# Kernel optimization log

Hardware: AMD Instinct MI355X
Metric: run time of the kernel (lower is better)

Reference implementation:

```python
import jax, jax.numpy as jnp
import numpy as np
from jax import lax

R = 8  # REGION_NUM_

def _avgpool3(x):
    # AvgPool2d(kernel=H-2*(H//3), stride=H//3) -> exactly 3x3 spatial output
    H = x.shape[2]
    s = H // 3
    k = H - 2 * s
    y = lax.reduce_window(x, 0.0, lax.add, (1, 1, k, k), (1, 1, s, s), 'VALID')
    return y / float(k * k)

def _hist_drconv(x, hist, wa, ba, wb, bb, out_ch):
    # x: [B,Cin,H,W], hist: [B,R,H,W]
    B, Cin, H, W = x.shape
    p = _avgpool3(x)                                                     # [B,Cin,3,3]
    h = jax.nn.sigmoid(jnp.einsum('bchw,oc->bohw', p, wa) + ba[None, :, None, None])  # [B,R*R,3,3]
    hg = h.reshape(B, R, R, 3, 3)
    wbg = wb.reshape(R, Cin * out_ch, R)                                 # grouped 1x1 conv, groups=R
    kern = jnp.einsum('brchw,roc->brohw', hg, wbg) + bb.reshape(1, R, Cin * out_ch, 1, 1)
    ki = kern.reshape(B, R * out_ch, Cin, 3, 3)                          # per-sample dynamic kernels
    def per_sample(xi, kb):
        # xi: [Cin,H,W], kb: [R*out,Cin,3,3] -> [R*out,H,W]
        return lax.conv_general_dilated(xi[None], kb, (1, 1), [(1, 1), (1, 1)])[0]
    y = jax.vmap(per_sample)(x, ki)                                      # [B,R*out,H,W]
    y = y.reshape(B, R, out_ch, H, W)
    # asign_index: one-hot of argmax over regions, select-sum
    mask = jax.nn.one_hot(jnp.argmax(hist, axis=1), R, axis=1, dtype=y.dtype)  # [B,R,H,W]
    return (y * mask[:, :, None]).sum(axis=1)                            # [B,out,H,W]

def _bn_relu(y, g, b, m, v):
    scale = (g / jnp.sqrt(v + 1e-5))[None, :, None, None]
    return jax.nn.relu((y - m[None, :, None, None]) * scale + b[None, :, None, None])

def setup_inputs() -> dict:
    key = jax.random.key(0)
    ks = jax.random.split(key, 20)
    B, Cin, Cmid, Cout, H = 8, 8, 8, 8, 256
    f32 = jnp.float32
    d = {}
    d['x'] = jax.random.normal(ks[0], (B, Cin, H, H), f32)
    d['histmap'] = jax.random.uniform(ks[1], (B, R, H, H), dtype=f32)
    d['w1a'] = jax.random.normal(ks[2], (R * R, Cin), f32) * 0.1
    d['b1a'] = jax.random.normal(ks[3], (R * R,), f32) * 0.1
    d['w1b'] = jax.random.normal(ks[4], (R * Cin * Cmid, R), f32) * 0.1
    d['b1b'] = jax.random.normal(ks[5], (R * Cin * Cmid,), f32) * 0.1
    d['g1'] = jax.random.uniform(ks[6], (Cmid,), dtype=f32) + 0.5
    d['be1'] = jax.random.normal(ks[7], (Cmid,), f32) * 0.1
    d['m1'] = jax.random.normal(ks[8], (Cmid,), f32) * 0.1
    d['v1'] = jax.random.uniform(ks[9], (Cmid,), dtype=f32) + 0.5
    d['w2a'] = jax.random.normal(ks[10], (R * R, Cmid), f32) * 0.1
    d['b2a'] = jax.random.normal(ks[11], (R * R,), f32) * 0.1
    d['w2b'] = jax.random.normal(ks[12], (R * Cmid * Cout, R), f32) * 0.1
    d['b2b'] = jax.random.normal(ks[13], (R * Cmid * Cout,), f32) * 0.1
    d['g2'] = jax.random.uniform(ks[14], (Cout,), dtype=f32) + 0.5
    d['be2'] = jax.random.normal(ks[15], (Cout,), f32) * 0.1
    d['m2'] = jax.random.normal(ks[16], (Cout,), f32) * 0.1
    d['v2'] = jax.random.uniform(ks[17], (Cout,), dtype=f32) + 0.5
    return d

def reference(x, histmap, w1a, b1a, w1b, b1b, g1, be1, m1, v1,
              w2a, b2a, w2b, b2b, g2, be2, m2, v2):
    y = _hist_drconv(x, histmap, w1a, b1a, w1b, b1b, 8)
    y = _bn_relu(y, g1, be1, m1, v1)
    y = _hist_drconv(y, histmap, w2a, b2a, w2b, b2b, 8)
    return _bn_relu(y, g2, be2, m2, v2)
```

## Files before the change

kernel.cpp:

```cpp
#include <hip/hip_runtime.h>
#include <math.h>


#define HWPX 65536
#define HDIM 256

typedef __fp16 h2 __attribute__((ext_vector_type(2)));

#if defined(__has_builtin) && __has_builtin(__builtin_amdgcn_fdot2)
__device__ __forceinline__ float fdot2(h2 a, h2 b, float c) {
  return __builtin_amdgcn_fdot2(a, b, c, false);
}
#else
__device__ __forceinline__ float fdot2(h2 a, h2 b, float c) {
  return c + (float)a[0] * (float)b[0] + (float)a[1] * (float)b[1];
}
#endif

union UH { uint u; h2 h; };
union U4H { uint4 u4; h2 h[4]; };

__global__ __launch_bounds__(256) void prep_kernel(const float* __restrict__ x,
                                                   const float* __restrict__ hist,
                                                   float* __restrict__ rs1,
                                                   uint* __restrict__ xh,
                                                   unsigned char* __restrict__ regmap) {
  int u = blockIdx.x;
  int t = threadIdx.x;
  int wave = t >> 6, lane = t & 63;
  if (u < 2048) {
    int cp = u & 3, rg = (u >> 2) & 63, b = u >> 8;
    int row = rg * 4 + wave;
    const float* pa = x + ((size_t)(b * 8 + 2 * cp) * HWPX) + row * HDIM + lane * 4;
    const float4 va = *(const float4*)pa;
    const float4 vb = *(const float4*)(pa + HWPX);
    U4H pk;
    pk.h[0] = __builtin_amdgcn_cvt_pkrtz(va.x, vb.x);
    pk.h[1] = __builtin_amdgcn_cvt_pkrtz(va.y, vb.y);
    pk.h[2] = __builtin_amdgcn_cvt_pkrtz(va.z, vb.z);
    pk.h[3] = __builtin_amdgcn_cvt_pkrtz(va.w, vb.w);
    *(uint4*)(xh + (size_t)(b * 4 + cp) * HWPX + row * HDIM + lane * 4) = pk.u4;
    float a0 = 0.f, a1 = 0.f, a2 = 0.f, b0 = 0.f, b1 = 0.f, b2 = 0.f;
#pragma unroll
    for (int p = 0; p < 4; p++) {
      int px = lane * 4 + p;
      float fa = (&va.x)[p], fb = (&vb.x)[p];
      if (px <= 85)  { a0 += fa; b0 += fb; }
      if (px >= 85 && px <= 170) { a1 += fa; b1 += fb; }
      if (px >= 170) { a2 += fa; b2 += fb; }
    }
#pragma unroll
    for (int off = 32; off >= 1; off >>= 1) {
      a0 += __shfl_xor(a0, off); a1 += __shfl_xor(a1, off); a2 += __shfl_xor(a2, off);
      b0 += __shfl_xor(b0, off); b1 += __shfl_xor(b1, off); b2 += __shfl_xor(b2, off);
    }
    if (lane == 0) {
      float* qa = rs1 + ((size_t)(b * 8 + 2 * cp) * 256 + row) * 3;
      qa[0] = a0; qa[1] = a1; qa[2] = a2;
      float* qb = qa + 768;
      qb[0] = b0; qb[1] = b1; qb[2] = b2;
    }
  } else {
    int u2 = u - 2048;
    int b = u2 >> 6, rg = u2 & 63;
    int row = rg * 4 + wave;
    int x0 = lane * 4;
    const float* hp = hist + (size_t)b * 8 * HWPX + row * HDIM + x0;
    float4 hv[8];
#pragma unroll
    for (int r = 0; r < 8; r++) hv[r] = *(const float4*)(hp + (size_t)r * HWPX);
    uchar4 rg4;
#pragma unroll
    for (int p = 0; p < 4; p++) {
      float best = (&hv[0].x)[p];
      int reg = 0;
#pragma unroll
      for (int r = 1; r < 8; r++) {
        float q = (&hv[r].x)[p];
        if (q > best) { best = q; reg = r; }
      }
      (&rg4.x)[p] = (unsigned char)reg;
    }
    *(uchar4*)(regmap + (size_t)b * HWPX + row * HDIM + x0) = rg4;
  }
}

template <int LAYER>
__global__ __launch_bounds__(256) void conv_kernel(
    const uint* __restrict__ xh, const unsigned char* __restrict__ regmap,
    const float* __restrict__ rs,
    const float* __restrict__ wa, const float* __restrict__ ba,
    const float* __restrict__ wb, const float* __restrict__ bb,
    const float* __restrict__ g, const float* __restrict__ be,
    const float* __restrict__ m, const float* __restrict__ v,
    uint* __restrict__ outh, float* __restrict__ outf,
    float* __restrict__ rs2out) {
  __shared__ uint KsU[8 * 292];
  __shared__ float pp[72][3];
  __shared__ float pP[8][9];
  __shared__ float hh[576];
  __shared__ float bns[8], bnsh[8];

  int bid = blockIdx.x;
  int b = bid & 7;
  int rg = bid >> 3;
  int wave = threadIdx.x >> 6, lane = threadIdx.x & 63;
  int row = rg * 4 + wave;
  int x0 = lane * 4;
  int t = threadIdx.x;

  if (t < 216) {
    int u = t / 3, part = t - 3 * (t / 3);
    int c = u / 9, ij = u % 9, i = ij / 3, j = ij % 3;
    int r0 = 85 * i + part * 29;
    int cnt = (part == 2) ? 28 : 29;
    const float* q = rs + ((size_t)(b * 8 + c) * 256 + r0) * 3 + j;
    float s = 0.f;
    for (int k = 0; k < cnt; k++) s += q[k * 3];
    pp[u][part] = s;
  }
  if (t >= 248) {
    int oc = t - 248;
    float s = g[oc] * rsqrtf(v[oc] + 1e-5f);
    bns[oc] = s;
    bnsh[oc] = be[oc] - m[oc] * s;
  }
  __syncthreads();
  if (t < 72) pP[t / 9][t % 9] = (pp[t][0] + pp[t][1] + pp[t][2]) * (1.f / 7396.f);
  __syncthreads();
  for (int u = t; u < 576; u += 256) {
    int o = u / 9, ij = u - o * 9;
    float z = ba[o];
#pragma unroll
    for (int c = 0; c < 8; c++) z += pP[c][ij] * wa[o * 8 + c];
    hh[u] = 1.f / (1.f + expf(-z));
  }
  __syncthreads();
  {
    int reg = t >> 5, z = t & 31, oc = z >> 2, q = z & 3;
    int row0 = reg * 64 + oc * 8 + q * 2;
    const float* w0p = wb + row0 * 8;
    float4 wA  = *(const float4*)(w0p);
    float4 wA2 = *(const float4*)(w0p + 4);
    float4 wB  = *(const float4*)(w0p + 8);
    float4 wB2 = *(const float4*)(w0p + 12);
    float bb0 = bb[row0], bb1 = bb[row0 + 1];
    const float* hp = hh + reg * 72;
#pragma unroll
    for (int tap = 0; tap < 9; tap++) {
      float v0 = bb0, v1 = bb1;
#pragma unroll
      for (int cc = 0; cc < 4; cc++) {
        float hv = hp[cc * 9 + tap];
        v0 += hv * (&wA.x)[cc];
        v1 += hv * (&wB.x)[cc];
      }
#pragma unroll
      for (int cc = 0; cc < 4; cc++) {
        float hv = hp[(4 + cc) * 9 + tap];
        v0 += hv * (&wA2.x)[cc];
        v1 += hv * (&wB2.x)[cc];
      }
      UH pk;
      pk.h[0] = (__fp16)v0;
      pk.h[1] = (__fp16)v1;
      KsU[reg * 292 + tap * 32 + z] = pk.u;
    }
  }
  __syncthreads();

  uint win[4][3][6];
#pragma unroll
  for (int cp = 0; cp < 4; cp++) {
    const uint* plane = xh + (size_t)(b * 4 + cp) * HWPX;
#pragma unroll
    for (int dy = 0; dy < 3; dy++) {
      int yy = row + dy - 1;
      if ((unsigned)yy < 256u) {
        const uint* rp = plane + yy * HDIM + x0;
        uint4 mv = *(const uint4*)rp;
        win[cp][dy][0] = (x0 > 0) ? rp[-1] : 0u;
        win[cp][dy][1] = mv.x; win[cp][dy][2] = mv.y;
        win[cp][dy][3] = mv.z; win[cp][dy][4] = mv.w;
        win[cp][dy][5] = (x0 < 252) ? rp[4] : 0u;
      } else {
#pragma unroll
        for (int q = 0; q < 6; q++) win[cp][dy][q] = 0u;
      }
    }
  }

  uchar4 rg4 = *(const uchar4*)(regmap + (size_t)b * HWPX + row * HDIM + x0);

  float acc[4][8];
#pragma unroll
  for (int p = 0; p < 4; p++)
#pragma unroll
    for (int oc = 0; oc < 8; oc++) acc[p][oc] = 0.f;

#pragma unroll
  for (int p = 0; p < 4; p++) {
    int reg = (&rg4.x)[p];
    const char* Kr = (const char*)KsU + reg * 1168;
#pragma unroll
    for (int di = 0; di < 3; di++) {
#pragma unroll
      for (int dj = 0; dj < 3; dj++) {
        UH w0, w1, w2, w3;
        w0.u = win[0][di][p + dj];
        w1.u = win[1][di][p + dj];
        w2.u = win[2][di][p + dj];
        w3.u = win[3][di][p + dj];
        const char* kt = Kr + (di * 3 + dj) * 128;
#pragma unroll
        for (int oc = 0; oc < 8; oc++) {
          U4H kw;
          kw.u4 = *(const uint4*)(kt + oc * 16);
          float a = acc[p][oc];
          a = fdot2(w0.h, kw.h[0], a);
          a = fdot2(w1.h, kw.h[1], a);
          a = fdot2(w2.h, kw.h[2], a);
          a = fdot2(w3.h, kw.h[3], a);
          acc[p][oc] = a;
        }
      }
    }
  }

#pragma unroll
  for (int p = 0; p < 4; p++)
#pragma unroll
    for (int oc = 0; oc < 8; oc++)
      acc[p][oc] = fmaxf(acc[p][oc] * bns[oc] + bnsh[oc], 0.f);

  if (LAYER == 1) {
#pragma unroll
    for (int cp = 0; cp < 4; cp++) {
      U4H pk;
#pragma unroll
      for (int p = 0; p < 4; p++)
        pk.h[p] = __builtin_amdgcn_cvt_pkrtz(acc[p][2 * cp], acc[p][2 * cp + 1]);
      *(uint4*)(outh + (size_t)(b * 4 + cp) * HWPX + row * HDIM + x0) = pk.u4;
    }
#pragma unroll
    for (int oc = 0; oc < 8; oc++) {
      float s0 = 0.f, s1 = 0.f, s2 = 0.f;
#pragma unroll
      for (int p = 0; p < 4; p++) {
        int px = x0 + p;
        float val = acc[p][oc];
        if (px <= 85) s0 += val;
        if (px >= 85 && px <= 170) s1 += val;
        if (px >= 170) s2 += val;
      }
#pragma unroll
      for (int off = 32; off >= 1; off >>= 1) {
        s0 += __shfl_xor(s0, off);
        s1 += __shfl_xor(s1, off);
        s2 += __shfl_xor(s2, off);
      }
      if (lane == 0) {
        float* q = rs2out + ((size_t)(b * 8 + oc) * 256 + row) * 3;
        q[0] = s0; q[1] = s1; q[2] = s2;
      }
    }
  } else {
#pragma unroll
    for (int oc = 0; oc < 8; oc++) {
      float4 o4 = make_float4(acc[0][oc], acc[1][oc], acc[2][oc], acc[3][oc]);
      *(float4*)(outf + (size_t)(b * 8 + oc) * HWPX + row * HDIM + x0) = o4;
    }
  }
}

extern "C" void kernel_launch(void* const* d_in, const int* in_sizes, int n_in,
                              void* d_out, int out_size, void* d_ws, size_t ws_size,
                              hipStream_t stream) {
  const float* x    = (const float*)d_in[0];
  const float* hist = (const float*)d_in[1];
  const float* w1a  = (const float*)d_in[2];
  const float* b1a  = (const float*)d_in[3];
  const float* w1b  = (const float*)d_in[4];
  const float* b1b  = (const float*)d_in[5];
  const float* g1   = (const float*)d_in[6];
  const float* be1  = (const float*)d_in[7];
  const float* m1   = (const float*)d_in[8];
  const float* v1   = (const float*)d_in[9];
  const float* w2a  = (const float*)d_in[10];
  const float* b2a  = (const float*)d_in[11];
  const float* w2b  = (const float*)d_in[12];
  const float* b2b  = (const float*)d_in[13];
  const float* g2   = (const float*)d_in[14];
  const float* be2  = (const float*)d_in[15];
  const float* m2   = (const float*)d_in[16];
  const float* v2   = (const float*)d_in[17];
  float* outp = (float*)d_out;

  char* ws = (char*)d_ws;
  unsigned char* regmap = (unsigned char*)ws;
  uint* xh  = (uint*)(ws + 524288);
  uint* y1h = (uint*)(ws + 8912896);
  float* rs1 = (float*)(ws + 17301504);
  float* rs2 = (float*)(ws + 17399808);

  prep_kernel<<<2560, 256, 0, stream>>>(x, hist, rs1, xh, regmap);
  conv_kernel<1><<<512, 256, 0, stream>>>(xh, regmap, rs1, w1a, b1a, w1b, b1b,
                                          g1, be1, m1, v1, y1h, nullptr, rs2);
  conv_kernel<2><<<512, 256, 0, stream>>>(y1h, regmap, rs2, w2a, b2a, w2b, b2b,
                                          g2, be2, m2, v2, nullptr, outp, nullptr);
}
```

Before: 55.72 us.

## Fuse prep and both conv layers into one persistent kernel with grid barriers

Merges the three launches into a single persistent kernel of 512 blocks that loops over the prep work, then runs layer-1 and layer-2 convolution phases separated by atomic-counter grid barriers. The goal is to remove kernel launch gaps and the tail drain between dependent stages. It adds a memset launch for the barrier counters and relies on all 512 blocks being co-resident, which an ordinary launch does not guarantee. Barrier spinning and fewer prep blocks in flight could also cost time.

```diff
diff --git a/kernel.cpp b/kernel.cpp
--- a/kernel.cpp
+++ b/kernel.cpp
@@ -4,6 +4,7 @@
 
 #define HWPX 65536
 #define HDIM 256
+#define NBLK 512u
 
 typedef __fp16 h2 __attribute__((ext_vector_type(2)));
 
@@ -20,13 +21,31 @@
 union UH { uint u; h2 h; };
 union U4H { uint4 u4; h2 h[4]; };
 
-__global__ __launch_bounds__(256) void prep_kernel(const float* __restrict__ x,
-                                                   const float* __restrict__ hist,
-                                                   float* __restrict__ rs1,
-                                                   uint* __restrict__ xh,
-                                                   unsigned char* __restrict__ regmap) {
-  int u = blockIdx.x;
-  int t = threadIdx.x;
+struct ConvSmem {
+  uint KsU[8 * 292];
+  float pp[72][3];
+  float pP[8][9];
+  float hh[576];
+  float bns[8], bnsh[8];
+};
+
+__device__ __forceinline__ void gridbar(uint* cnt, uint target) {
+  __syncthreads();
+  if (threadIdx.x == 0) {
+    __threadfence();
+    atomicAdd(cnt, 1u);
+    while (atomicAdd(cnt, 0u) < target) __builtin_amdgcn_s_sleep(8);
+  }
+  __syncthreads();
+  __threadfence();
+}
+
+__device__ __forceinline__ void prep_unit(int u, int t,
+                                          const float* __restrict__ x,
+                                          const float* __restrict__ hist,
+                                          float* __restrict__ rs1,
+                                          uint* __restrict__ xh,
+                                          unsigned char* __restrict__ regmap) {
   int wave = t >> 6, lane = t & 63;
   if (u < 2048) {
     int cp = u & 3, rg = (u >> 2) & 63, b = u >> 8;
@@ -86,7 +105,8 @@
 }
 
 template <int LAYER>
-__global__ __launch_bounds__(256) void conv_kernel(
+__device__ __forceinline__ void conv_phase(
+    ConvSmem& sm, int bid, int t,
     const uint* __restrict__ xh, const unsigned char* __restrict__ regmap,
     const float* __restrict__ rs,
     const float* __restrict__ wa, const float* __restrict__ ba,
@@ -95,19 +115,11 @@
     const float* __restrict__ m, const float* __restrict__ v,
     uint* __restrict__ outh, float* __restrict__ outf,
     float* __restrict__ rs2out) {
-  __shared__ uint KsU[8 * 292];
-  __shared__ float pp[72][3];
-  __shared__ float pP[8][9];
-  __shared__ float hh[576];
-  __shared__ float bns[8], bnsh[8];
-
-  int bid = blockIdx.x;
   int b = bid & 7;
   int rg = bid >> 3;
-  int wave = threadIdx.x >> 6, lane = threadIdx.x & 63;
+  int wave = t >> 6, lane = t & 63;
   int row = rg * 4 + wave;
   int x0 = lane * 4;
-  int t = threadIdx.x;
 
   if (t < 216) {
     int u = t / 3, part = t - 3 * (t / 3);
@@ -117,23 +129,23 @@
     const float* q = rs + ((size_t)(b * 8 + c) * 256 + r0) * 3 + j;
     float s = 0.f;
     for (int k = 0; k < cnt; k++) s += q[k * 3];
-    pp[u][part] = s;
+    sm.pp[u][part] = s;
   }
   if (t >= 248) {
     int oc = t - 248;
     float s = g[oc] * rsqrtf(v[oc] + 1e-5f);
-    bns[oc] = s;
-    bnsh[oc] = be[oc] - m[oc] * s;
-  }
-  __syncthreads();
-  if (t < 72) pP[t / 9][t % 9] = (pp[t][0] + pp[t][1] + pp[t][2]) * (1.f / 7396.f);
+    sm.bns[oc] = s;
+    sm.bnsh[oc] = be[oc] - m[oc] * s;
+  }
+  __syncthreads();
+  if (t < 72) sm.pP[t / 9][t % 9] = (sm.pp[t][0] + sm.pp[t][1] + sm.pp[t][2]) * (1.f / 7396.f);
   __syncthreads();
   for (int u = t; u < 576; u += 256) {
     int o = u / 9, ij = u - o * 9;
     float z = ba[o];
 #pragma unroll
-    for (int c = 0; c < 8; c++) z += pP[c][ij] * wa[o * 8 + c];
-    hh[u] = 1.f / (1.f + expf(-z));
+    for (int c = 0; c < 8; c++) z += sm.pP[c][ij] * wa[o * 8 + c];
+    sm.hh[u] = 1.f / (1.f + expf(-z));
   }
   __syncthreads();
   {
@@ -145,7 +157,7 @@
     float4 wB  = *(const float4*)(w0p + 8);
     float4 wB2 = *(const float4*)(w0p + 12);
     float bb0 = bb[row0], bb1 = bb[row0 + 1];
-    const float* hp = hh + reg * 72;
+    const float* hp = sm.hh + reg * 72;
 #pragma unroll
     for (int tap = 0; tap < 9; tap++) {
       float v0 = bb0, v1 = bb1;
@@ -164,7 +176,7 @@
       UH pk;
       pk.h[0] = (__fp16)v0;
       pk.h[1] = (__fp16)v1;
-      KsU[reg * 292 + tap * 32 + z] = pk.u;
+      sm.KsU[reg * 292 + tap * 32 + z] = pk.u;
     }
   }
   __syncthreads();
@@ -201,7 +213,7 @@
 #pragma unroll
   for (int p = 0; p < 4; p++) {
     int reg = (&rg4.x)[p];
-    const char* Kr = (const char*)KsU + reg * 1168;
+    const char* Kr = (const char*)sm.KsU + reg * 1168;
 #pragma unroll
     for (int di = 0; di < 3; di++) {
 #pragma unroll
@@ -231,7 +243,7 @@
   for (int p = 0; p < 4; p++)
 #pragma unroll
     for (int oc = 0; oc < 8; oc++)
-      acc[p][oc] = fmaxf(acc[p][oc] * bns[oc] + bnsh[oc], 0.f);
+      acc[p][oc] = fmaxf(acc[p][oc] * sm.bns[oc] + sm.bnsh[oc], 0.f);
 
   if (LAYER == 1) {
 #pragma unroll
@@ -271,6 +283,33 @@
       *(float4*)(outf + (size_t)(b * 8 + oc) * HWPX + row * HDIM + x0) = o4;
     }
   }
+}
+
+__global__ __launch_bounds__(256, 2) void fused_kernel(
+    const float* __restrict__ x, const float* __restrict__ hist,
+    const float* __restrict__ w1a, const float* __restrict__ b1a,
+    const float* __restrict__ w1b, const float* __restrict__ b1b,
+    const float* __restrict__ g1, const float* __restrict__ be1,
+    const float* __restrict__ m1, const float* __restrict__ v1,
+    const float* __restrict__ w2a, const float* __restrict__ b2a,
+    const float* __restrict__ w2b, const float* __restrict__ b2b,
+    const float* __restrict__ g2, const float* __restrict__ be2,
+    const float* __restrict__ m2, const float* __restrict__ v2,
+    float* __restrict__ outp, unsigned char* __restrict__ regmap,
+    uint* __restrict__ xh, uint* __restrict__ y1h,
+    float* __restrict__ rs1, float* __restrict__ rs2,
+    uint* __restrict__ bar) {
+  __shared__ ConvSmem sm;
+  int bid = blockIdx.x;
+  int t = threadIdx.x;
+
+  for (int u = bid; u < 2560; u += 512) prep_unit(u, t, x, hist, rs1, xh, regmap);
+  gridbar(bar + 0, NBLK);
+  conv_phase<1>(sm, bid, t, xh, regmap, rs1, w1a, b1a, w1b, b1b,
+                g1, be1, m1, v1, y1h, nullptr, rs2);
+  gridbar(bar + 16, NBLK);
+  conv_phase<2>(sm, bid, t, y1h, regmap, rs2, w2a, b2a, w2b, b2b,
+                g2, be2, m2, v2, nullptr, outp, nullptr);
 }
 
 extern "C" void kernel_launch(void* const* d_in, const int* in_sizes, int n_in,
@@ -302,10 +341,18 @@
   uint* y1h = (uint*)(ws + 8912896);
   float* rs1 = (float*)(ws + 17301504);
   float* rs2 = (float*)(ws + 17399808);
-
-  prep_kernel<<<2560, 256, 0, stream>>>(x, hist, rs1, xh, regmap);
-  conv_kernel<1><<<512, 256, 0, stream>>>(xh, regmap, rs1, w1a, b1a, w1b, b1b,
-                                          g1, be1, m1, v1, y1h, nullptr, rs2);
-  conv_kernel<2><<<512, 256, 0, stream>>>(y1h, regmap, rs2, w2a, b2a, w2b, b2b,
-                                          g2, be2, m2, v2, nullptr, outp, nullptr);
-}
+  uint* bar  = (uint*)(ws + 17498112);
+
+  hipMemsetAsync(bar, 0, 128, stream);
+
+  void* args[] = {
+    (void*)&x, (void*)&hist,
+    (void*)&w1a, (void*)&b1a, (void*)&w1b, (void*)&b1b,
+    (void*)&g1, (void*)&be1, (void*)&m1, (void*)&v1,
+    (void*)&w2a, (void*)&b2a, (void*)&w2b, (void*)&b2b,
+    (void*)&g2, (void*)&be2, (void*)&m2, (void*)&v2,
+    (void*)&outp, (void*)&regmap, (void*)&xh, (void*)&y1h,
+    (void*)&rs1, (void*)&rs2, (void*)&bar,
+  };
+  hipLaunchKernel((const void*)fused_kernel, dim3(512), dim3(256), args, 0, stream);
+}
```

Result: slower. 191.7 us (+244.1%).

## Halve per-thread pixels, double conv grid, and hoist window loads before kernel build

Applied to the files above, without the earlier changes.

Each thread now computes 2 pixels instead of 4, with two waves covering a row, so the conv grid doubles to 1024 blocks and occupancy should rise under launch_bounds(256,4). The input-window and region-map loads move ahead of the per-block dynamic-kernel construction so their latency overlaps that setup work. Row-sum partials from the two half-row waves are combined through shared memory. The cost is that each block rebuilds its dynamic kernels for half as many pixels, doubling that redundant setup overall.

```diff
diff --git a/kernel.cpp b/kernel.cpp
--- a/kernel.cpp
+++ b/kernel.cpp
@@ -86,7 +86,7 @@
 }
 
 template <int LAYER>
-__global__ __launch_bounds__(256) void conv_kernel(
+__global__ __launch_bounds__(256, 4) void conv_kernel(
     const uint* __restrict__ xh, const unsigned char* __restrict__ regmap,
     const float* __restrict__ rs,
     const float* __restrict__ wa, const float* __restrict__ ba,
@@ -100,14 +100,38 @@
   __shared__ float pP[8][9];
   __shared__ float hh[576];
   __shared__ float bns[8], bnsh[8];
+  __shared__ float wred[4][8][3];
 
   int bid = blockIdx.x;
   int b = bid & 7;
   int rg = bid >> 3;
-  int wave = threadIdx.x >> 6, lane = threadIdx.x & 63;
-  int row = rg * 4 + wave;
-  int x0 = lane * 4;
   int t = threadIdx.x;
+  int wave = t >> 6, lane = t & 63;
+  int row = rg * 2 + (wave >> 1);
+  int x0 = (wave & 1) * 128 + lane * 2;
+
+  uint win[4][3][4];
+#pragma unroll
+  for (int cp = 0; cp < 4; cp++) {
+    const uint* plane = xh + (size_t)(b * 4 + cp) * HWPX;
+#pragma unroll
+    for (int dy = 0; dy < 3; dy++) {
+      int yy = row + dy - 1;
+      if ((unsigned)yy < 256u) {
+        const uint* rp = plane + yy * HDIM + x0;
+        uint2 mv = *(const uint2*)rp;
+        win[cp][dy][0] = (x0 > 0) ? rp[-1] : 0u;
+        win[cp][dy][1] = mv.x;
+        win[cp][dy][2] = mv.y;
+        win[cp][dy][3] = (x0 < 254) ? rp[2] : 0u;
+      } else {
+#pragma unroll
+        for (int q = 0; q < 4; q++) win[cp][dy][q] = 0u;
+      }
+    }
+  }
+  const unsigned char* rmp = regmap + (size_t)b * HWPX + row * HDIM + x0;
+  int reg0 = rmp[0], reg1 = rmp[1];
 
   if (t < 216) {
     int u = t / 3, part = t - 3 * (t / 3);
@@ -169,38 +193,15 @@
   }
   __syncthreads();
 
-  uint win[4][3][6];
-#pragma unroll
-  for (int cp = 0; cp < 4; cp++) {
-    const uint* plane = xh + (size_t)(b * 4 + cp) * HWPX;
-#pragma unroll
-    for (int dy = 0; dy < 3; dy++) {
-      int yy = row + dy - 1;
-      if ((unsigned)yy < 256u) {
-        const uint* rp = plane + yy * HDIM + x0;
-        uint4 mv = *(const uint4*)rp;
-        win[cp][dy][0] = (x0 > 0) ? rp[-1] : 0u;
-        win[cp][dy][1] = mv.x; win[cp][dy][2] = mv.y;
-        win[cp][dy][3] = mv.z; win[cp][dy][4] = mv.w;
-        win[cp][dy][5] = (x0 < 252) ? rp[4] : 0u;
-      } else {
-#pragma unroll
-        for (int q = 0; q < 6; q++) win[cp][dy][q] = 0u;
-      }
-    }
-  }
-
-  uchar4 rg4 = *(const uchar4*)(regmap + (size_t)b * HWPX + row * HDIM + x0);
-
-  float acc[4][8];
-#pragma unroll
-  for (int p = 0; p < 4; p++)
+  float acc[2][8];
+#pragma unroll
+  for (int p = 0; p < 2; p++)
 #pragma unroll
     for (int oc = 0; oc < 8; oc++) acc[p][oc] = 0.f;
 
 #pragma unroll
-  for (int p = 0; p < 4; p++) {
-    int reg = (&rg4.x)[p];
+  for (int p = 0; p < 2; p++) {
+    int reg = p ? reg1 : reg0;
     const char* Kr = (const char*)KsU + reg * 1168;
 #pragma unroll
     for (int di = 0; di < 3; di++) {
@@ -228,7 +229,7 @@
   }
 
 #pragma unroll
-  for (int p = 0; p < 4; p++)
+  for (int p = 0; p < 2; p++)
 #pragma unroll
     for (int oc = 0; oc < 8; oc++)
       acc[p][oc] = fmaxf(acc[p][oc] * bns[oc] + bnsh[oc], 0.f);
@@ -236,17 +237,18 @@
   if (LAYER == 1) {
 #pragma unroll
     for (int cp = 0; cp < 4; cp++) {
-      U4H pk;
-#pragma unroll
-      for (int p = 0; p < 4; p++)
-        pk.h[p] = __builtin_amdgcn_cvt_pkrtz(acc[p][2 * cp], acc[p][2 * cp + 1]);
-      *(uint4*)(outh + (size_t)(b * 4 + cp) * HWPX + row * HDIM + x0) = pk.u4;
+      uint2 pk;
+      UH h0, h1;
+      h0.h = __builtin_amdgcn_cvt_pkrtz(acc[0][2 * cp], acc[0][2 * cp + 1]);
+      h1.h = __builtin_amdgcn_cvt_pkrtz(acc[1][2 * cp], acc[1][2 * cp + 1]);
+      pk.x = h0.u; pk.y = h1.u;
+      *(uint2*)(outh + (size_t)(b * 4 + cp) * HWPX + row * HDIM + x0) = pk;
     }
 #pragma unroll
     for (int oc = 0; oc < 8; oc++) {
       float s0 = 0.f, s1 = 0.f, s2 = 0.f;
 #pragma unroll
-      for (int p = 0; p < 4; p++) {
+      for (int p = 0; p < 2; p++) {
         int px = x0 + p;
         float val = acc[p][oc];
         if (px <= 85) s0 += val;
@@ -259,16 +261,20 @@
         s1 += __shfl_xor(s1, off);
         s2 += __shfl_xor(s2, off);
       }
-      if (lane == 0) {
-        float* q = rs2out + ((size_t)(b * 8 + oc) * 256 + row) * 3;
-        q[0] = s0; q[1] = s1; q[2] = s2;
-      }
+      if (lane == 0) { wred[wave][oc][0] = s0; wred[wave][oc][1] = s1; wred[wave][oc][2] = s2; }
+    }
+    __syncthreads();
+    if (t < 48) {
+      int row_sub = t / 24, rem = t - row_sub * 24;
+      int oc = rem / 3, j = rem - 3 * oc;
+      float s = wred[row_sub * 2][oc][j] + wred[row_sub * 2 + 1][oc][j];
+      rs2out[((size_t)(b * 8 + oc) * 256 + (rg * 2 + row_sub)) * 3 + j] = s;
     }
   } else {
 #pragma unroll
     for (int oc = 0; oc < 8; oc++) {
-      float4 o4 = make_float4(acc[0][oc], acc[1][oc], acc[2][oc], acc[3][oc]);
-      *(float4*)(outf + (size_t)(b * 8 + oc) * HWPX + row * HDIM + x0) = o4;
+      float2 o2 = make_float2(acc[0][oc], acc[1][oc]);
+      *(float2*)(outf + (size_t)(b * 8 + oc) * HWPX + row * HDIM + x0) = o2;
     }
   }
 }
@@ -304,8 +310,8 @@
   float* rs2 = (float*)(ws + 17399808);
 
   prep_kernel<<<2560, 256, 0, stream>>>(x, hist, rs1, xh, regmap);
-  conv_kernel<1><<<512, 256, 0, stream>>>(xh, regmap, rs1, w1a, b1a, w1b, b1b,
-                                          g1, be1, m1, v1, y1h, nullptr, rs2);
-  conv_kernel<2><<<512, 256, 0, stream>>>(y1h, regmap, rs2, w2a, b2a, w2b, b2b,
-                                          g2, be2, m2, v2, nullptr, outp, nullptr);
-}
+  conv_kernel<1><<<1024, 256, 0, stream>>>(xh, regmap, rs1, w1a, b1a, w1b, b1b,
+                                           g1, be1, m1, v1, y1h, nullptr, rs2);
+  conv_kernel<2><<<1024, 256, 0, stream>>>(y1h, regmap, rs2, w2a, b2a, w2b, b2b,
+                                           g2, be2, m2, v2, nullptr, outp, nullptr);
+}
```

After: 62.78 us. +12.7%, slower.

## Compute dynamic region conv with MFMA over all regions and select via LDS

Applied to the files above, without the earlier changes.

Activations move to a channel-interleaved NHWC fp16 layout (8 channels per 16-byte word), and the conv kernel now stages six input rows in shared memory. Each wave then runs the 3x3 conv as an implicit GEMM with 16x16x32 f16 MFMA across all 64 region×channel outputs, picking the per-pixel region's outputs from an LDS staging buffer. This trades per-pixel fdot2 loops for matrix-core throughput at the cost of computing all 8 regions (8x redundant FLOPs) plus extra LDS traffic. The prep kernel now packs all 8 channels per block, and layer-2 output stores become scalar per pixel.

```diff
diff --git a/kernel.cpp b/kernel.cpp
--- a/kernel.cpp
+++ b/kernel.cpp
@@ -5,66 +5,63 @@
 #define HWPX 65536
 #define HDIM 256
 
-typedef __fp16 h2 __attribute__((ext_vector_type(2)));
-
-#if defined(__has_builtin) && __has_builtin(__builtin_amdgcn_fdot2)
-__device__ __forceinline__ float fdot2(h2 a, h2 b, float c) {
-  return __builtin_amdgcn_fdot2(a, b, c, false);
-}
-#else
-__device__ __forceinline__ float fdot2(h2 a, h2 b, float c) {
-  return c + (float)a[0] * (float)b[0] + (float)a[1] * (float)b[1];
-}
-#endif
-
-union UH { uint u; h2 h; };
-union U4H { uint4 u4; h2 h[4]; };
+typedef __fp16 h2v __attribute__((ext_vector_type(2)));
+typedef __fp16 v8h __attribute__((ext_vector_type(8)));
+typedef float v4f __attribute__((ext_vector_type(4)));
+
+union UH { uint u; h2v h; };
+union U4V8 { uint4 u4; v8h h8; };
 
 __global__ __launch_bounds__(256) void prep_kernel(const float* __restrict__ x,
                                                    const float* __restrict__ hist,
                                                    float* __restrict__ rs1,
-                                                   uint* __restrict__ xh,
+                                                   uint4* __restrict__ xh4,
                                                    unsigned char* __restrict__ regmap) {
-  int u = blockIdx.x;
-  int t = threadIdx.x;
-  int wave = t >> 6, lane = t & 63;
-  if (u < 2048) {
-    int cp = u & 3, rg = (u >> 2) & 63, b = u >> 8;
-    int row = rg * 4 + wave;
-    const float* pa = x + ((size_t)(b * 8 + 2 * cp) * HWPX) + row * HDIM + lane * 4;
-    const float4 va = *(const float4*)pa;
-    const float4 vb = *(const float4*)(pa + HWPX);
-    U4H pk;
-    pk.h[0] = __builtin_amdgcn_cvt_pkrtz(va.x, vb.x);
-    pk.h[1] = __builtin_amdgcn_cvt_pkrtz(va.y, vb.y);
-    pk.h[2] = __builtin_amdgcn_cvt_pkrtz(va.z, vb.z);
-    pk.h[3] = __builtin_amdgcn_cvt_pkrtz(va.w, vb.w);
-    *(uint4*)(xh + (size_t)(b * 4 + cp) * HWPX + row * HDIM + lane * 4) = pk.u4;
-    float a0 = 0.f, a1 = 0.f, a2 = 0.f, b0 = 0.f, b1 = 0.f, b2 = 0.f;
+  int u = blockIdx.x, t = threadIdx.x, w = t >> 6, l = t & 63;
+  if (u < 512) {
+    int b = u & 7, rg = u >> 3;
+    int row = rg * 4 + w;
+    const float* base = x + (size_t)b * 8 * HWPX + row * HDIM + l * 4;
+    float4 ch[8];
+#pragma unroll
+    for (int c = 0; c < 8; c++) ch[c] = *(const float4*)(base + (size_t)c * HWPX);
+    uint4* dst = xh4 + ((size_t)b * 256 + row) * 256 + l * 4;
 #pragma unroll
     for (int p = 0; p < 4; p++) {
-      int px = lane * 4 + p;
-      float fa = (&va.x)[p], fb = (&vb.x)[p];
-      if (px <= 85)  { a0 += fa; b0 += fb; }
-      if (px >= 85 && px <= 170) { a1 += fa; b1 += fb; }
-      if (px >= 170) { a2 += fa; b2 += fb; }
-    }
-#pragma unroll
-    for (int off = 32; off >= 1; off >>= 1) {
-      a0 += __shfl_xor(a0, off); a1 += __shfl_xor(a1, off); a2 += __shfl_xor(a2, off);
-      b0 += __shfl_xor(b0, off); b1 += __shfl_xor(b1, off); b2 += __shfl_xor(b2, off);
-    }
-    if (lane == 0) {
-      float* qa = rs1 + ((size_t)(b * 8 + 2 * cp) * 256 + row) * 3;
-      qa[0] = a0; qa[1] = a1; qa[2] = a2;
-      float* qb = qa + 768;
-      qb[0] = b0; qb[1] = b1; qb[2] = b2;
+      UH h0, h1, h2, h3;
+      h0.h = __builtin_amdgcn_cvt_pkrtz((&ch[0].x)[p], (&ch[1].x)[p]);
+      h1.h = __builtin_amdgcn_cvt_pkrtz((&ch[2].x)[p], (&ch[3].x)[p]);
+      h2.h = __builtin_amdgcn_cvt_pkrtz((&ch[4].x)[p], (&ch[5].x)[p]);
+      h3.h = __builtin_amdgcn_cvt_pkrtz((&ch[6].x)[p], (&ch[7].x)[p]);
+      dst[p] = make_uint4(h0.u, h1.u, h2.u, h3.u);
+    }
+#pragma unroll
+    for (int c = 0; c < 8; c++) {
+      float s0 = 0.f, s1 = 0.f, s2 = 0.f;
+#pragma unroll
+      for (int p = 0; p < 4; p++) {
+        int px = l * 4 + p;
+        float val = (&ch[c].x)[p];
+        if (px <= 85) s0 += val;
+        if (px >= 85 && px <= 170) s1 += val;
+        if (px >= 170) s2 += val;
+      }
+#pragma unroll
+      for (int off = 32; off >= 1; off >>= 1) {
+        s0 += __shfl_xor(s0, off);
+        s1 += __shfl_xor(s1, off);
+        s2 += __shfl_xor(s2, off);
+      }
+      if (l == 0) {
+        float* q = rs1 + ((size_t)(b * 8 + c) * 256 + row) * 3;
+        q[0] = s0; q[1] = s1; q[2] = s2;
+      }
     }
   } else {
-    int u2 = u - 2048;
-    int b = u2 >> 6, rg = u2 & 63;
-    int row = rg * 4 + wave;
-    int x0 = lane * 4;
+    int u2 = u - 512;
+    int b = u2 & 7, rg = u2 >> 3;
+    int row = rg * 4 + w;
+    int x0 = l * 4;
     const float* hp = hist + (size_t)b * 8 * HWPX + row * HDIM + x0;
     float4 hv[8];
 #pragma unroll
@@ -86,8 +83,8 @@
 }
 
 template <int LAYER>
-__global__ __launch_bounds__(256) void conv_kernel(
-    const uint* __restrict__ xh, const unsigned char* __restrict__ regmap,
+__global__ __launch_bounds__(256, 2) void conv_kernel(
+    const uint4* __restrict__ in4, const unsigned char* __restrict__ regmap,
     const float* __restrict__ rs,
     const float* __restrict__ wa, const float* __restrict__ ba,
     const float* __restrict__ wb, const float* __restrict__ bb,
@@ -95,26 +92,38 @@
     const float* __restrict__ m, const float* __restrict__ v,
     uint* __restrict__ outh, float* __restrict__ outf,
     float* __restrict__ rs2out) {
-  __shared__ uint KsU[8 * 292];
+  __shared__ uint4 xs[6][260];
+  __shared__ __align__(16) float Dbuf[4][64][20];
+  __shared__ uint4 Bf[4][3][64];
   __shared__ float pp[72][3];
   __shared__ float pP[8][9];
   __shared__ float hh[576];
   __shared__ float bns[8], bnsh[8];
+  __shared__ unsigned char rm[4][256];
 
   int bid = blockIdx.x;
-  int b = bid & 7;
-  int rg = bid >> 3;
-  int wave = threadIdx.x >> 6, lane = threadIdx.x & 63;
-  int row = rg * 4 + wave;
-  int x0 = lane * 4;
-  int t = threadIdx.x;
+  int b = bid & 7, rg = bid >> 3, r0 = rg * 4;
+  int t = threadIdx.x, w = t >> 6, l = t & 63;
+
+  for (int i = t; i < 6 * 256; i += 256) {
+    int dy = i >> 8, px = i & 255;
+    int yy = r0 - 1 + dy;
+    uint4 val = make_uint4(0, 0, 0, 0);
+    if ((unsigned)yy < 256u) val = in4[((size_t)b * 256 + yy) * 256 + px];
+    xs[dy][px + 1] = val;
+  }
+  if (t < 12) {
+    int rr = t % 6, cc = (t < 6) ? 0 : 257;
+    xs[rr][cc] = make_uint4(0, 0, 0, 0);
+  }
+  ((uint*)rm)[t] = *(const uint*)(regmap + (size_t)b * HWPX + (r0 + (t >> 6)) * HDIM + (t & 63) * 4);
 
   if (t < 216) {
     int u = t / 3, part = t - 3 * (t / 3);
     int c = u / 9, ij = u % 9, i = ij / 3, j = ij % 3;
-    int r0 = 85 * i + part * 29;
+    int rr0 = 85 * i + part * 29;
     int cnt = (part == 2) ? 28 : 29;
-    const float* q = rs + ((size_t)(b * 8 + c) * 256 + r0) * 3 + j;
+    const float* q = rs + ((size_t)(b * 8 + c) * 256 + rr0) * 3 + j;
     float s = 0.f;
     for (int k = 0; k < cnt; k++) s += q[k * 3];
     pp[u][part] = s;
@@ -137,138 +146,111 @@
   }
   __syncthreads();
   {
-    int reg = t >> 5, z = t & 31, oc = z >> 2, q = z & 3;
-    int row0 = reg * 64 + oc * 8 + q * 2;
-    const float* w0p = wb + row0 * 8;
-    float4 wA  = *(const float4*)(w0p);
-    float4 wA2 = *(const float4*)(w0p + 4);
-    float4 wB  = *(const float4*)(w0p + 8);
-    float4 wB2 = *(const float4*)(w0p + 12);
-    float bb0 = bb[row0], bb1 = bb[row0 + 1];
-    const float* hp = hh + reg * 72;
-#pragma unroll
-    for (int tap = 0; tap < 9; tap++) {
-      float v0 = bb0, v1 = bb1;
-#pragma unroll
-      for (int cc = 0; cc < 4; cc++) {
-        float hv = hp[cc * 9 + tap];
-        v0 += hv * (&wA.x)[cc];
-        v1 += hv * (&wB.x)[cc];
-      }
-#pragma unroll
-      for (int cc = 0; cc < 4; cc++) {
-        float hv = hp[(4 + cc) * 9 + tap];
-        v0 += hv * (&wA2.x)[cc];
-        v1 += hv * (&wB2.x)[cc];
-      }
+    int nt = t >> 6, l2 = t & 63;
+    int n = nt * 16 + (l2 & 15);
+    int reg = n >> 3, oc = n & 7;
+#pragma unroll
+    for (int ks = 0; ks < 3; ks++) {
+      int tap = ks * 4 + (l2 >> 4);
+      uint4 rec = make_uint4(0, 0, 0, 0);
+      if (tap < 9) {
+        float hv[8];
+#pragma unroll
+        for (int cc = 0; cc < 8; cc++) hv[cc] = hh[(reg * 8 + cc) * 9 + tap];
+        float vj[8];
+#pragma unroll
+        for (int j = 0; j < 8; j++) {
+          int rowk = reg * 64 + oc * 8 + j;
+          float val = bb[rowk];
+#pragma unroll
+          for (int cc = 0; cc < 8; cc++) val += hv[cc] * wb[rowk * 8 + cc];
+          vj[j] = val;
+        }
+        UH p0, p1, p2, p3;
+        p0.h = __builtin_amdgcn_cvt_pkrtz(vj[0], vj[1]);
+        p1.h = __builtin_amdgcn_cvt_pkrtz(vj[2], vj[3]);
+        p2.h = __builtin_amdgcn_cvt_pkrtz(vj[4], vj[5]);
+        p3.h = __builtin_amdgcn_cvt_pkrtz(vj[6], vj[7]);
+        rec = make_uint4(p0.u, p1.u, p2.u, p3.u);
+      }
+      Bf[nt][ks][l2] = rec;
+    }
+  }
+  __syncthreads();
+
+  U4V8 Bfr[4][3];
+#pragma unroll
+  for (int nt = 0; nt < 4; nt++)
+#pragma unroll
+    for (int ks = 0; ks < 3; ks++)
+      Bfr[nt][ks].u4 = Bf[nt][ks][l];
+
+  int row = r0 + w;
+  int ocp = l >> 4;
+  float bn_s0 = bns[2 * ocp], bn_h0 = bnsh[2 * ocp];
+  float bn_s1 = bns[2 * ocp + 1], bn_h1 = bnsh[2 * ocp + 1];
+  float rsm[2][3] = {{0.f, 0.f, 0.f}, {0.f, 0.f, 0.f}};
+
+  for (int mt = 0; mt < 16; mt++) {
+    U4V8 A[3];
+#pragma unroll
+    for (int ks = 0; ks < 3; ks++) {
+      int tap = ks * 4 + (l >> 4);
+      if (tap > 8) tap = 8;
+      int dy = tap / 3, dx = tap - dy * 3;
+      A[ks].u4 = xs[w + dy][mt * 16 + (l & 15) + dx];
+    }
+    v4f acc[4];
+#pragma unroll
+    for (int nt = 0; nt < 4; nt++) {
+      v4f z = {0.f, 0.f, 0.f, 0.f};
+      z = __builtin_amdgcn_mfma_f32_16x16x32_f16(A[0].h8, Bfr[nt][0].h8, z, 0, 0, 0);
+      z = __builtin_amdgcn_mfma_f32_16x16x32_f16(A[1].h8, Bfr[nt][1].h8, z, 0, 0, 0);
+      z = __builtin_amdgcn_mfma_f32_16x16x32_f16(A[2].h8, Bfr[nt][2].h8, z, 0, 0, 0);
+      acc[nt] = z;
+    }
+#pragma unroll
+    for (int nt = 0; nt < 4; nt++) {
+      int col = nt * 16 + (l & 15);
+      int px0 = (l >> 4) * 4;
+      *(v4f*)&Dbuf[w][col][px0] = acc[nt];
+    }
+    int gx = l & 15;
+    int px = mt * 16 + gx;
+    int reg = rm[w][px];
+    int c0 = reg * 8 + ocp * 2;
+    float o0 = Dbuf[w][c0][gx];
+    float o1 = Dbuf[w][c0 + 1][gx];
+    o0 = fmaxf(o0 * bn_s0 + bn_h0, 0.f);
+    o1 = fmaxf(o1 * bn_s1 + bn_h1, 0.f);
+    if (LAYER == 1) {
       UH pk;
-      pk.h[0] = (__fp16)v0;
-      pk.h[1] = (__fp16)v1;
-      KsU[reg * 292 + tap * 32 + z] = pk.u;
-    }
-  }
-  __syncthreads();
-
-  uint win[4][3][6];
-#pragma unroll
-  for (int cp = 0; cp < 4; cp++) {
-    const uint* plane = xh + (size_t)(b * 4 + cp) * HWPX;
-#pragma unroll
-    for (int dy = 0; dy < 3; dy++) {
-      int yy = row + dy - 1;
-      if ((unsigned)yy < 256u) {
-        const uint* rp = plane + yy * HDIM + x0;
-        uint4 mv = *(const uint4*)rp;
-        win[cp][dy][0] = (x0 > 0) ? rp[-1] : 0u;
-        win[cp][dy][1] = mv.x; win[cp][dy][2] = mv.y;
-        win[cp][dy][3] = mv.z; win[cp][dy][4] = mv.w;
-        win[cp][dy][5] = (x0 < 252) ? rp[4] : 0u;
-      } else {
-#pragma unroll
-        for (int q = 0; q < 6; q++) win[cp][dy][q] = 0u;
-      }
-    }
-  }
-
-  uchar4 rg4 = *(const uchar4*)(regmap + (size_t)b * HWPX + row * HDIM + x0);
-
-  float acc[4][8];
-#pragma unroll
-  for (int p = 0; p < 4; p++)
-#pragma unroll
-    for (int oc = 0; oc < 8; oc++) acc[p][oc] = 0.f;
-
-#pragma unroll
-  for (int p = 0; p < 4; p++) {
-    int reg = (&rg4.x)[p];
-    const char* Kr = (const char*)KsU + reg * 1168;
-#pragma unroll
-    for (int di = 0; di < 3; di++) {
-#pragma unroll
-      for (int dj = 0; dj < 3; dj++) {
-        UH w0, w1, w2, w3;
-        w0.u = win[0][di][p + dj];
-        w1.u = win[1][di][p + dj];
-        w2.u = win[2][di][p + dj];
-        w3.u = win[3][di][p + dj];
-        const char* kt = Kr + (di * 3 + dj) * 128;
-#pragma unroll
-        for (int oc = 0; oc < 8; oc++) {
-          U4H kw;
-          kw.u4 = *(const uint4*)(kt + oc * 16);
-          float a = acc[p][oc];
-          a = fdot2(w0.h, kw.h[0], a);
-          a = fdot2(w1.h, kw.h[1], a);
-          a = fdot2(w2.h, kw.h[2], a);
-          a = fdot2(w3.h, kw.h[3], a);
-          acc[p][oc] = a;
-        }
-      }
-    }
-  }
-
-#pragma unroll
-  for (int p = 0; p < 4; p++)
-#pragma unroll
-    for (int oc = 0; oc < 8; oc++)
-      acc[p][oc] = fmaxf(acc[p][oc] * bns[oc] + bnsh[oc], 0.f);
+      pk.h = __builtin_amdgcn_cvt_pkrtz(o0, o1);
+      outh[(((size_t)b * 256 + row) * 256 + px) * 4 + ocp] = pk.u;
+      if (px <= 85)               { rsm[0][0] += o0; rsm[1][0] += o1; }
+      if (px >= 85 && px <= 170)  { rsm[0][1] += o0; rsm[1][1] += o1; }
+      if (px >= 170)              { rsm[0][2] += o0; rsm[1][2] += o1; }
+    } else {
+      outf[((size_t)(b * 8 + 2 * ocp)) * HWPX + row * HDIM + px] = o0;
+      outf[((size_t)(b * 8 + 2 * ocp + 1)) * HWPX + row * HDIM + px] = o1;
+    }
+  }
 
   if (LAYER == 1) {
 #pragma unroll
-    for (int cp = 0; cp < 4; cp++) {
-      U4H pk;
-#pragma unroll
-      for (int p = 0; p < 4; p++)
-        pk.h[p] = __builtin_amdgcn_cvt_pkrtz(acc[p][2 * cp], acc[p][2 * cp + 1]);
-      *(uint4*)(outh + (size_t)(b * 4 + cp) * HWPX + row * HDIM + x0) = pk.u4;
-    }
-#pragma unroll
-    for (int oc = 0; oc < 8; oc++) {
-      float s0 = 0.f, s1 = 0.f, s2 = 0.f;
-#pragma unroll
-      for (int p = 0; p < 4; p++) {
-        int px = x0 + p;
-        float val = acc[p][oc];
-        if (px <= 85) s0 += val;
-        if (px >= 85 && px <= 170) s1 += val;
-        if (px >= 170) s2 += val;
-      }
-#pragma unroll
-      for (int off = 32; off >= 1; off >>= 1) {
-        s0 += __shfl_xor(s0, off);
-        s1 += __shfl_xor(s1, off);
-        s2 += __shfl_xor(s2, off);
-      }
-      if (lane == 0) {
-        float* q = rs2out + ((size_t)(b * 8 + oc) * 256 + row) * 3;
-        q[0] = s0; q[1] = s1; q[2] = s2;
-      }
-    }
-  } else {
-#pragma unroll
-    for (int oc = 0; oc < 8; oc++) {
-      float4 o4 = make_float4(acc[0][oc], acc[1][oc], acc[2][oc], acc[3][oc]);
-      *(float4*)(outf + (size_t)(b * 8 + oc) * HWPX + row * HDIM + x0) = o4;
+    for (int i = 0; i < 2; i++)
+#pragma unroll
+      for (int j = 0; j < 3; j++) {
+#pragma unroll
+        for (int off = 1; off <= 8; off <<= 1)
+          rsm[i][j] += __shfl_xor(rsm[i][j], off);
+      }
+    if ((l & 15) == 0) {
+#pragma unroll
+      for (int i = 0; i < 2; i++) {
+        float* q = rs2out + ((size_t)(b * 8 + 2 * ocp + i) * 256 + row) * 3;
+        q[0] = rsm[i][0]; q[1] = rsm[i][1]; q[2] = rsm[i][2];
+      }
     }
   }
 }
@@ -298,14 +280,14 @@
 
   char* ws = (char*)d_ws;
   unsigned char* regmap = (unsigned char*)ws;
-  uint* xh  = (uint*)(ws + 524288);
-  uint* y1h = (uint*)(ws + 8912896);
+  uint4* xh4  = (uint4*)(ws + 524288);
+  uint4* y1h4 = (uint4*)(ws + 8912896);
   float* rs1 = (float*)(ws + 17301504);
   float* rs2 = (float*)(ws + 17399808);
 
-  prep_kernel<<<2560, 256, 0, stream>>>(x, hist, rs1, xh, regmap);
-  conv_kernel<1><<<512, 256, 0, stream>>>(xh, regmap, rs1, w1a, b1a, w1b, b1b,
-                                          g1, be1, m1, v1, y1h, nullptr, rs2);
-  conv_kernel<2><<<512, 256, 0, stream>>>(y1h, regmap, rs2, w2a, b2a, w2b, b2b,
+  prep_kernel<<<1024, 256, 0, stream>>>(x, hist, rs1, xh4, regmap);
+  conv_kernel<1><<<512, 256, 0, stream>>>(xh4, regmap, rs1, w1a, b1a, w1b, b1b,
+                                          g1, be1, m1, v1, (uint*)y1h4, nullptr, rs2);
+  conv_kernel<2><<<512, 256, 0, stream>>>(y1h4, regmap, rs2, w2a, b2a, w2b, b2b,
                                           g2, be2, m2, v2, nullptr, outp, nullptr);
 }
```

After: 65.27 us. 1.17x slower.
